# Performance work log

Measured on AMD Instinct MI355X. Metric: run time of the kernel, lower is better.

## Reference

```python
import jax, jax.numpy as jnp
import numpy as np
from jax import lax

# config (matches init_kwargs)
A, M, S, SR, L = 4, 32, 48000, 48000, 16000
NB = 8        # len(f_range)
BIN = 64      # alpha/beta bins (hardcoded in original)
TWO_PI = 2.0 * np.pi
NON_LINEAR_RATE = 0.3   # forward arg non_linear_rate
NOISE_RATE = 0.0        # forward arg noise_rate -> noise branch is a no-op
LOG10 = np.float32(np.log(10.0))

F_VALUES = jnp.asarray(np.geomspace(20.0, 8000.0, NB), jnp.float32)
ALPHA_VALUES = jnp.asarray(np.exp(np.linspace(np.log(3.0 / 10.0), np.log(3.0 * 100.0), BIN)), jnp.float32)
BETA_VALUES = jnp.asarray(np.exp(np.linspace(np.log(1e-9 / 10.0), np.log(1e-9 * 100.0), BIN)), jnp.float32)


def weighted_sum(params, values):
    # softplus -> normalize over last dim -> convex-ish combination of `values`
    x = jax.nn.softplus(params)
    x = x / x.sum(axis=-1, keepdims=True)
    return (x * values).sum(axis=-1)


def modified_sigmoid(x):
    # DDSP-style modified sigmoid used by DirectValue
    return 2.0 * jax.nn.sigmoid(x) ** LOG10 + 1e-7


def setup_inputs() -> dict:
    key = jax.random.key(0)
    ks = jax.random.split(key, 6)
    u = lambda k, shape, lo, hi: jax.random.uniform(k, shape, jnp.float32, lo, hi)
    return {
        "freq_lin_p": u(ks[0], (1, M, 1, NB), -4.0, 4.0),
        "freq_nl_p": u(ks[1], (A, M, S, NB), -4.0, 4.0),
        "alpha_p": u(ks[2], (1, M, 1, BIN), -4.0, 4.0),
        "beta_p": u(ks[3], (1, M, 1, BIN), -4.0, 4.0),
        "amp_v": u(ks[4], (A, M, 1), 0.0, 0.04),
        "forces": jax.random.normal(ks[5], (A, L), jnp.float32),
    }


def reference(freq_lin_p, freq_nl_p, alpha_p, beta_p, amp_v, forces):
    amp = modified_sigmoid(amp_v)                                   # [A,M,1]
    f_lin = weighted_sum(freq_lin_p, F_VALUES)                      # [1,M,1]
    undamped = f_lin + NON_LINEAR_RATE * weighted_sum(freq_nl_p, F_VALUES)  # [A,M,S]
    lbd = (undamped * TWO_PI) ** 2                                  # [A,M,S]
    alpha = weighted_sum(alpha_p, ALPHA_VALUES)                     # [1,M,1]
    beta = weighted_sum(beta_p, BETA_VALUES)                        # [1,M,1]
    damp = 0.5 * (alpha + beta * lbd)                               # [A,M,S]
    freq = jnp.sqrt(lbd - damp ** 2) / TWO_PI                       # [A,M,S]
    cum_damp = jnp.cumsum(damp / SR, axis=2)
    cum_freq = jnp.cumsum(freq / SR, axis=2)
    signal = (amp * jnp.exp(-cum_damp) * jnp.sin(TWO_PI * cum_freq)).sum(axis=1)  # [A,S]
    # grouped conv1d with time-flipped forces == full convolution with forces
    kernel = jnp.flip(forces, axis=-1)[:, None, :]                  # [A,1,L] (OIH)
    out = lax.conv_general_dilated(
        signal[None],                                               # [1,A,S]
        kernel,
        window_strides=(1,),
        padding=[(L - 1, L - 1)],
        feature_group_count=A,
        dimension_numbers=("NCH", "OIH", "NCH"),
    )
    out = out[0, :, :S]                                             # [A,S]
    return out  # + noise * NOISE_RATE (NOISE_RATE == 0)
```

## Files before the change

kernel.cpp:

```cpp
#include <hip/hip_runtime.h>
#include <hip/hip_bf16.h>
#include <math.h>

#define A_ 4
#define M_ 32
#define S_ 48000
#define L_ 16000
#define NB_ 8
#define BIN_ 64
#define TWO_PI_F 6.28318530717958647692f
#define INV_SR (1.0f / 48000.0f)
#define NCHUNK 47
#define NROW 128
#define SBPAD 16000
#define SBLEN 64256
#define SB_PLANE 257024
#define NKT 501
#define FB_PLANE 1026048u
#define UT_PER_A 188

#define CST_OFF    0u
#define SIG_OFF    1024u
#define PART_OFF   769024u
#define SIGBF_OFF  865280u
#define FRAGB_OFF  1893376u
#define WS_NEEDED  5997568u

typedef __attribute__((ext_vector_type(8))) short bf16x8;
typedef __attribute__((ext_vector_type(4))) float f32x4;

__device__ __forceinline__ float softplusf(float x) {
    float t = __expf(-fabsf(x));
    return fmaxf(x, 0.f) + __logf(1.f + t);
}
__device__ __forceinline__ unsigned short bfbits(float v) {
    __hip_bfloat16 h = __float2bfloat16(v);
    return *(unsigned short*)&h;
}
__device__ __forceinline__ float bf2f(unsigned short u) {
    unsigned x = ((unsigned)u) << 16;
    return *(float*)&x;
}

__global__ void k_precompute(const float* __restrict__ flin_p,
                             const float* __restrict__ alpha_p,
                             const float* __restrict__ beta_p,
                             const float* __restrict__ amp_v,
                             float* __restrict__ cst) {
    __shared__ float sF[NB_], sA[BIN_], sB[BIN_];
    int tid = threadIdx.x;
    if (tid < NB_) {
        double lf = log(20.0) + (double)tid * ((log(8000.0) - log(20.0)) / 7.0);
        float v = (float)exp(lf);
        sF[tid] = v; cst[tid] = v;
    }
    if (tid < BIN_) {
        double la = log(0.3) + (double)tid * ((log(300.0) - log(0.3)) / 63.0);
        sA[tid] = (float)exp(la);
        double lb = log(1e-10) + (double)tid * ((log(1e-7) - log(1e-10)) / 63.0);
        sB[tid] = (float)exp(lb);
    }
    __syncthreads();
    if (tid < M_) {
        float sum = 0.f, dot = 0.f;
        for (int i = 0; i < NB_; ++i) {
            float sp = softplusf(flin_p[tid * NB_ + i]);
            sum += sp; dot = fmaf(sp, sF[i], dot);
        }
        cst[8 + tid] = dot / sum;
        sum = 0.f; dot = 0.f;
        for (int i = 0; i < BIN_; ++i) {
            float sp = softplusf(alpha_p[tid * BIN_ + i]);
            sum += sp; dot = fmaf(sp, sA[i], dot);
        }
        cst[40 + tid] = dot / sum;
        sum = 0.f; dot = 0.f;
        for (int i = 0; i < BIN_; ++i) {
            float sp = softplusf(beta_p[tid * BIN_ + i]);
            sum += sp; dot = fmaf(sp, sB[i], dot);
        }
        cst[72 + tid] = dot / sum;
    }
    if (tid < A_ * M_) {
        float x = amp_v[tid];
        float sg = 1.f / (1.f + __expf(-x));
        cst[104 + tid] = 2.f * __expf(2.30258509299404568402f * __logf(sg)) + 1e-7f;
    }
}

__global__ __launch_bounds__(256) void k_fragB(const float* __restrict__ forces,
                                               unsigned short* __restrict__ fragB) {
    int t = blockIdx.x * 256 + threadIdx.x;
    if (t >= A_ * NKT * 64) return;
    int l  = t & 63;
    int kk = (t >> 6) % NKT;
    int a  = t / (NKT * 64);
    int v  = l & 15, hq = l >> 4;
    unsigned short hi[8], lo[8];
#pragma unroll
    for (int j = 0; j < 8; ++j) {
        int k = hq * 8 + j;
        int r = k & 15, hw = k >> 4;
        int fj = 32 * kk + 16 * hw + v - r;
        float fv = (fj >= 0 && fj < L_) ? forces[a * L_ + fj] : 0.f;
        hi[j] = bfbits(fv);
        lo[j] = bfbits(fv - bf2f(hi[j]));
    }
    uint4 ph, pl;
    ph.x = (unsigned)hi[0] | ((unsigned)hi[1] << 16);
    ph.y = (unsigned)hi[2] | ((unsigned)hi[3] << 16);
    ph.z = (unsigned)hi[4] | ((unsigned)hi[5] << 16);
    ph.w = (unsigned)hi[6] | ((unsigned)hi[7] << 16);
    pl.x = (unsigned)lo[0] | ((unsigned)lo[1] << 16);
    pl.y = (unsigned)lo[2] | ((unsigned)lo[3] << 16);
    pl.z = (unsigned)lo[4] | ((unsigned)lo[5] << 16);
    pl.w = (unsigned)lo[6] | ((unsigned)lo[7] << 16);
    ((uint4*)fragB)[t] = ph;
    ((uint4*)fragB)[FB_PLANE / 8 + t] = pl;
}

__device__ __forceinline__ void inc_partials(const float4* __restrict__ nl4,
                                             const float* __restrict__ cst,
                                             int row, int s0,
                                             float* lpx, float* lpy,
                                             float& rx, float& ry) {
    int m = row & 31;
    float Fv[8];
#pragma unroll
    for (int i = 0; i < 8; ++i) Fv[i] = cst[i];
    float flin = cst[8 + m], al = cst[40 + m], be = cst[72 + m];
    rx = 0.f; ry = 0.f;
#pragma unroll
    for (int k = 0; k < 4; ++k) {
        int s = s0 + k;
        float vx = 0.f, vy = 0.f;
        if (s < S_) {
            size_t off = ((size_t)row * S_ + s) * 2;
            float4 x0 = nl4[off];
            float4 x1 = nl4[off + 1];
            float xs[8] = {x0.x, x0.y, x0.z, x0.w, x1.x, x1.y, x1.z, x1.w};
            float sum = 0.f, dot = 0.f;
#pragma unroll
            for (int i = 0; i < 8; ++i) {
                float sp = softplusf(xs[i]);
                sum += sp; dot = fmaf(sp, Fv[i], dot);
            }
            float und = flin + 0.3f * (dot / sum);
            float w = TWO_PI_F * und;
            float lbd = w * w;
            float damp = 0.5f * fmaf(be, lbd, al);
            float freq = sqrtf(lbd - damp * damp) * (1.0f / TWO_PI_F);
            vx = damp * INV_SR;
            vy = freq * INV_SR;
        }
        rx += vx; lpx[k] = rx;
        ry += vy; lpy[k] = ry;
    }
}

__global__ __launch_bounds__(256) void k_sum(const float* __restrict__ nl,
                                             const float* __restrict__ cst,
                                             double2* __restrict__ part) {
    int chunk = blockIdx.x, row = blockIdx.y, tid = threadIdx.x;
    float lpx[4], lpy[4], rx, ry;
    inc_partials((const float4*)nl, cst, row, chunk * 1024 + tid * 4, lpx, lpy, rx, ry);

    __shared__ double rd[256], rf[256];
    rd[tid] = (double)rx; rf[tid] = (double)ry;
    __syncthreads();
    for (int o = 128; o > 0; o >>= 1) {
        if (tid < o) { rd[tid] += rd[tid + o]; rf[tid] += rf[tid + o]; }
        __syncthreads();
    }
    if (tid == 0) {
        double2 p; p.x = rd[0]; p.y = rf[0];
        part[row * NCHUNK + chunk] = p;
    }
}

__global__ void k_phase2(double2* __restrict__ part) {
    int r = threadIdx.x;
    if (r < NROW) {
        double cx = 0.0, cy = 0.0;
        for (int c = 0; c < NCHUNK; ++c) {
            double2 t = part[r * NCHUNK + c];
            double2 e; e.x = cx; e.y = cy;
            part[r * NCHUNK + c] = e;
            cx += t.x; cy += t.y;
        }
    }
}

__global__ __launch_bounds__(256) void k_eval(const float* __restrict__ nl,
                                              const float* __restrict__ cst,
                                              const double2* __restrict__ part,
                                              float* __restrict__ sig) {
    int chunk = blockIdx.x, row = blockIdx.y, tid = threadIdx.x;
    int a = row >> 5;
    int s0 = chunk * 1024 + tid * 4;
    float lpx[4], lpy[4], rx, ry;
    inc_partials((const float4*)nl, cst, row, s0, lpx, lpy, rx, ry);

    double2 carry = part[row * NCHUNK + chunk];
    float amp = cst[104 + row];

    __shared__ double sx[256], sy[256];
    sx[tid] = (double)rx; sy[tid] = (double)ry;
    __syncthreads();
    for (int o = 1; o < 256; o <<= 1) {
        double ax = (tid >= o) ? sx[tid - o] : 0.0;
        double ay = (tid >= o) ? sy[tid - o] : 0.0;
        __syncthreads();
        sx[tid] += ax; sy[tid] += ay;
        __syncthreads();
    }
    double ex = ((tid > 0) ? sx[tid - 1] : 0.0) + carry.x;
    double ey = ((tid > 0) ? sy[tid - 1] : 0.0) + carry.y;

#pragma unroll
    for (int k = 0; k < 4; ++k) {
        int s = s0 + k;
        if (s < S_) {
            double cd = ex + (double)lpx[k];
            if (cd < 16.0) {
                double cf = ey + (double)lpy[k];
                float ph = (float)(cf - floor(cf));
                float val = amp * __expf(-(float)cd) * __sinf(TWO_PI_F * ph);
                atomicAdd(&sig[a * S_ + s], val);
            }
        }
    }
}

__global__ __launch_bounds__(256) void k_convert(const float* __restrict__ sig,
                                                 unsigned short* __restrict__ sigbf) {
    int i = blockIdx.x * 256 + threadIdx.x;
    if (i >= A_ * SBLEN) return;
    int a = i / SBLEN, p = i - a * SBLEN;
    int s = p - SBPAD;
    float v = (s >= 0 && s < S_) ? sig[a * S_ + s] : 0.f;
    unsigned short hi = bfbits(v);
    sigbf[i] = hi;
    sigbf[SB_PLANE + i] = bfbits(v - bf2f(hi));
}

__global__ __launch_bounds__(512) void k_conv(const unsigned short* __restrict__ sigbf,
                                              const unsigned short* __restrict__ fragB,
                                              float* __restrict__ out) {
    int tile = blockIdx.x;
    int a = tile / UT_PER_A, ut = tile - a * UT_PER_A;
    int u0 = ut * 16;
    int tid = threadIdx.x;
    int wv = tid >> 6;
    int l  = tid & 63;
    int du = l & 15, hq = l >> 4, hw = hq >> 1, hr = hq & 1;

    int nkk = (u0 >> 1) + 9;
    if (nkk > NKT) nkk = NKT;

    const unsigned short* sH = sigbf + (size_t)a * SBLEN;
    const unsigned short* sL = sH + SB_PLANE;
    int ebase = SBPAD + 16 * (u0 + du) - 16 * hw + 8 * hr;
    const unsigned short* fH = fragB + (((size_t)a * NKT) * 64 + l) * 8;
    const unsigned short* fL = fH + FB_PLANE;

    f32x4 acc0 = {0.f, 0.f, 0.f, 0.f};
    f32x4 acc1 = {0.f, 0.f, 0.f, 0.f};

    for (int kk = wv; kk < nkk; kk += 16) {
        {
            int e = ebase - 32 * kk;
            bf16x8 ah = *(const bf16x8*)(sH + e);
            bf16x8 al = *(const bf16x8*)(sL + e);
            bf16x8 bh = *(const bf16x8*)(fH + (size_t)kk * 512);
            bf16x8 bl = *(const bf16x8*)(fL + (size_t)kk * 512);
            acc0 = __builtin_amdgcn_mfma_f32_16x16x32_bf16(ah, bh, acc0, 0, 0, 0);
            acc0 = __builtin_amdgcn_mfma_f32_16x16x32_bf16(al, bh, acc0, 0, 0, 0);
            acc0 = __builtin_amdgcn_mfma_f32_16x16x32_bf16(ah, bl, acc0, 0, 0, 0);
        }
        int k2 = kk + 8;
        if (k2 < nkk) {
            int e = ebase - 32 * k2;
            bf16x8 ah = *(const bf16x8*)(sH + e);
            bf16x8 al = *(const bf16x8*)(sL + e);
            bf16x8 bh = *(const bf16x8*)(fH + (size_t)k2 * 512);
            bf16x8 bl = *(const bf16x8*)(fL + (size_t)k2 * 512);
            acc1 = __builtin_amdgcn_mfma_f32_16x16x32_bf16(ah, bh, acc1, 0, 0, 0);
            acc1 = __builtin_amdgcn_mfma_f32_16x16x32_bf16(al, bh, acc1, 0, 0, 0);
            acc1 = __builtin_amdgcn_mfma_f32_16x16x32_bf16(ah, bl, acc1, 0, 0, 0);
        }
    }
    acc0 = acc0 + acc1;

    __shared__ float red[8][256];
#pragma unroll
    for (int r = 0; r < 4; ++r)
        red[wv][(hq * 4 + r) * 16 + (l & 15)] = acc0[r];
    __syncthreads();

    if (tid < 256) {
        float s = 0.f;
#pragma unroll
        for (int w2 = 0; w2 < 8; ++w2) s += red[w2][tid];
        int t = u0 * 16 + tid;
        if (t < S_) out[(size_t)a * S_ + t] = s;
    }
}

extern "C" void kernel_launch(void* const* d_in, const int* in_sizes, int n_in,
                              void* d_out, int out_size, void* d_ws, size_t ws_size,
                              hipStream_t stream) {
    if (ws_size < (size_t)WS_NEEDED) return;

    const float* flin_p  = (const float*)d_in[0];
    const float* nl_p    = (const float*)d_in[1];
    const float* alpha_p = (const float*)d_in[2];
    const float* beta_p  = (const float*)d_in[3];
    const float* amp_v   = (const float*)d_in[4];
    const float* forces  = (const float*)d_in[5];
    float* out = (float*)d_out;

    char* ws = (char*)d_ws;
    float*          cst    = (float*)(ws + CST_OFF);
    float*          sig    = (float*)(ws + SIG_OFF);
    double2*        part   = (double2*)(ws + PART_OFF);
    unsigned short* sigbf  = (unsigned short*)(ws + SIGBF_OFF);
    unsigned short* fragB  = (unsigned short*)(ws + FRAGB_OFF);

    hipMemsetAsync(sig, 0, (size_t)A_ * S_ * sizeof(float), stream);

    hipLaunchKernelGGL(k_precompute, dim3(1), dim3(256), 0, stream,
                       flin_p, alpha_p, beta_p, amp_v, cst);
    hipLaunchKernelGGL(k_fragB, dim3(501), dim3(256), 0, stream, forces, fragB);
    hipLaunchKernelGGL(k_sum, dim3(NCHUNK, NROW), dim3(256), 0, stream,
                       nl_p, cst, part);
    hipLaunchKernelGGL(k_phase2, dim3(1), dim3(128), 0, stream, part);
    hipLaunchKernelGGL(k_eval, dim3(NCHUNK, NROW), dim3(256), 0, stream,
                       nl_p, cst, part, sig);
    hipLaunchKernelGGL(k_convert, dim3(1004), dim3(256), 0, stream, sig, sigbf);
    hipLaunchKernelGGL(k_conv, dim3(A_ * UT_PER_A), dim3(512), 0, stream,
                       sigbf, fragB, out);
}
```

Before: 446.8 us.

## Fuse scan into single-pass decoupled lookback, drop split-bf16, retile conv

Result: slower. 1.022 ms (+128.7%).

```diff
diff --git a/kernel.cpp b/kernel.cpp
--- a/kernel.cpp
+++ b/kernel.cpp
@@ -14,17 +14,20 @@
 #define NROW 128
 #define SBPAD 16000
 #define SBLEN 64256
-#define SB_PLANE 257024
 #define NKT 501
-#define FB_PLANE 1026048u
-#define UT_PER_A 188
+#define MB_ 64
+#define CB_PER_A 47
 
 #define CST_OFF    0u
 #define SIG_OFF    1024u
-#define PART_OFF   769024u
-#define SIGBF_OFF  865280u
-#define FRAGB_OFF  1893376u
-#define WS_NEEDED  5997568u
+#define SIGBF_OFF  769024u
+#define FRAGB_OFF  1283072u
+#define FLAG_OFF   3335168u
+#define AGGD_OFF   3359232u
+#define AGGF_OFF   3407360u
+#define INCLD_OFF  3455488u
+#define INCLF_OFF  3503616u
+#define WS_NEEDED  3551744u
 
 typedef __attribute__((ext_vector_type(8))) short bf16x8;
 typedef __attribute__((ext_vector_type(4))) float f32x4;
@@ -36,10 +39,6 @@
 __device__ __forceinline__ unsigned short bfbits(float v) {
     __hip_bfloat16 h = __float2bfloat16(v);
     return *(unsigned short*)&h;
-}
-__device__ __forceinline__ float bf2f(unsigned short u) {
-    unsigned x = ((unsigned)u) << 16;
-    return *(float*)&x;
 }
 
 __global__ void k_precompute(const float* __restrict__ flin_p,
@@ -96,7 +95,7 @@
     int kk = (t >> 6) % NKT;
     int a  = t / (NKT * 64);
     int v  = l & 15, hq = l >> 4;
-    unsigned short hi[8], lo[8];
+    unsigned short hi[8];
 #pragma unroll
     for (int j = 0; j < 8; ++j) {
         int k = hq * 8 + j;
@@ -104,32 +103,34 @@
         int fj = 32 * kk + 16 * hw + v - r;
         float fv = (fj >= 0 && fj < L_) ? forces[a * L_ + fj] : 0.f;
         hi[j] = bfbits(fv);
-        lo[j] = bfbits(fv - bf2f(hi[j]));
-    }
-    uint4 ph, pl;
+    }
+    uint4 ph;
     ph.x = (unsigned)hi[0] | ((unsigned)hi[1] << 16);
     ph.y = (unsigned)hi[2] | ((unsigned)hi[3] << 16);
     ph.z = (unsigned)hi[4] | ((unsigned)hi[5] << 16);
     ph.w = (unsigned)hi[6] | ((unsigned)hi[7] << 16);
-    pl.x = (unsigned)lo[0] | ((unsigned)lo[1] << 16);
-    pl.y = (unsigned)lo[2] | ((unsigned)lo[3] << 16);
-    pl.z = (unsigned)lo[4] | ((unsigned)lo[5] << 16);
-    pl.w = (unsigned)lo[6] | ((unsigned)lo[7] << 16);
     ((uint4*)fragB)[t] = ph;
-    ((uint4*)fragB)[FB_PLANE / 8 + t] = pl;
-}
-
-__device__ __forceinline__ void inc_partials(const float4* __restrict__ nl4,
-                                             const float* __restrict__ cst,
-                                             int row, int s0,
-                                             float* lpx, float* lpy,
-                                             float& rx, float& ry) {
-    int m = row & 31;
+}
+
+__global__ __launch_bounds__(256) void k_scan(const float* __restrict__ nl,
+                                              const float* __restrict__ cst,
+                                              float* __restrict__ sig,
+                                              double* aggd, double* aggf,
+                                              double* incld, double* inclf,
+                                              int* flags) {
+    int chunk = blockIdx.x, row = blockIdx.y, tid = threadIdx.x;
+    int m = row & 31, a = row >> 5;
+
     float Fv[8];
 #pragma unroll
     for (int i = 0; i < 8; ++i) Fv[i] = cst[i];
     float flin = cst[8 + m], al = cst[40 + m], be = cst[72 + m];
-    rx = 0.f; ry = 0.f;
+    float amp = cst[104 + row];
+
+    const float4* nl4 = (const float4*)nl;
+    int s0 = chunk * 1024 + tid * 4;
+    float lpx[4], lpy[4];
+    float rx = 0.f, ry = 0.f;
 #pragma unroll
     for (int k = 0; k < 4; ++k) {
         int s = s0 + k;
@@ -156,55 +157,9 @@
         rx += vx; lpx[k] = rx;
         ry += vy; lpy[k] = ry;
     }
-}
-
-__global__ __launch_bounds__(256) void k_sum(const float* __restrict__ nl,
-                                             const float* __restrict__ cst,
-                                             double2* __restrict__ part) {
-    int chunk = blockIdx.x, row = blockIdx.y, tid = threadIdx.x;
-    float lpx[4], lpy[4], rx, ry;
-    inc_partials((const float4*)nl, cst, row, chunk * 1024 + tid * 4, lpx, lpy, rx, ry);
-
-    __shared__ double rd[256], rf[256];
-    rd[tid] = (double)rx; rf[tid] = (double)ry;
-    __syncthreads();
-    for (int o = 128; o > 0; o >>= 1) {
-        if (tid < o) { rd[tid] += rd[tid + o]; rf[tid] += rf[tid + o]; }
-        __syncthreads();
-    }
-    if (tid == 0) {
-        double2 p; p.x = rd[0]; p.y = rf[0];
-        part[row * NCHUNK + chunk] = p;
-    }
-}
-
-__global__ void k_phase2(double2* __restrict__ part) {
-    int r = threadIdx.x;
-    if (r < NROW) {
-        double cx = 0.0, cy = 0.0;
-        for (int c = 0; c < NCHUNK; ++c) {
-            double2 t = part[r * NCHUNK + c];
-            double2 e; e.x = cx; e.y = cy;
-            part[r * NCHUNK + c] = e;
-            cx += t.x; cy += t.y;
-        }
-    }
-}
-
-__global__ __launch_bounds__(256) void k_eval(const float* __restrict__ nl,
-                                              const float* __restrict__ cst,
-                                              const double2* __restrict__ part,
-                                              float* __restrict__ sig) {
-    int chunk = blockIdx.x, row = blockIdx.y, tid = threadIdx.x;
-    int a = row >> 5;
-    int s0 = chunk * 1024 + tid * 4;
-    float lpx[4], lpy[4], rx, ry;
-    inc_partials((const float4*)nl, cst, row, s0, lpx, lpy, rx, ry);
-
-    double2 carry = part[row * NCHUNK + chunk];
-    float amp = cst[104 + row];
 
     __shared__ double sx[256], sy[256];
+    __shared__ double sPd, sPf;
     sx[tid] = (double)rx; sy[tid] = (double)ry;
     __syncthreads();
     for (int o = 1; o < 256; o <<= 1) {
@@ -214,9 +169,42 @@
         sx[tid] += ax; sy[tid] += ay;
         __syncthreads();
     }
-    double ex = ((tid > 0) ? sx[tid - 1] : 0.0) + carry.x;
-    double ey = ((tid > 0) ? sy[tid - 1] : 0.0) + carry.y;
-
+
+    if (tid == 0) {
+        int idx = row * NCHUNK + chunk;
+        double Td = sx[255], Tf = sy[255];
+        double Pd = 0.0, Pf = 0.0;
+        if (chunk == 0) {
+            __hip_atomic_store(&incld[idx], Td, __ATOMIC_RELAXED, __HIP_MEMORY_SCOPE_AGENT);
+            __hip_atomic_store(&inclf[idx], Tf, __ATOMIC_RELAXED, __HIP_MEMORY_SCOPE_AGENT);
+            __hip_atomic_store(&flags[idx], 2, __ATOMIC_RELEASE, __HIP_MEMORY_SCOPE_AGENT);
+        } else {
+            __hip_atomic_store(&aggd[idx], Td, __ATOMIC_RELAXED, __HIP_MEMORY_SCOPE_AGENT);
+            __hip_atomic_store(&aggf[idx], Tf, __ATOMIC_RELAXED, __HIP_MEMORY_SCOPE_AGENT);
+            __hip_atomic_store(&flags[idx], 1, __ATOMIC_RELEASE, __HIP_MEMORY_SCOPE_AGENT);
+            int i = idx - 1;
+            while (1) {
+                int fl = __hip_atomic_load(&flags[i], __ATOMIC_ACQUIRE, __HIP_MEMORY_SCOPE_AGENT);
+                if (fl == 0) { __builtin_amdgcn_s_sleep(1); continue; }
+                if (fl == 2) {
+                    Pd += __hip_atomic_load(&incld[i], __ATOMIC_RELAXED, __HIP_MEMORY_SCOPE_AGENT);
+                    Pf += __hip_atomic_load(&inclf[i], __ATOMIC_RELAXED, __HIP_MEMORY_SCOPE_AGENT);
+                    break;
+                }
+                Pd += __hip_atomic_load(&aggd[i], __ATOMIC_RELAXED, __HIP_MEMORY_SCOPE_AGENT);
+                Pf += __hip_atomic_load(&aggf[i], __ATOMIC_RELAXED, __HIP_MEMORY_SCOPE_AGENT);
+                --i;
+            }
+            __hip_atomic_store(&incld[idx], Pd + Td, __ATOMIC_RELAXED, __HIP_MEMORY_SCOPE_AGENT);
+            __hip_atomic_store(&inclf[idx], Pf + Tf, __ATOMIC_RELAXED, __HIP_MEMORY_SCOPE_AGENT);
+            __hip_atomic_store(&flags[idx], 2, __ATOMIC_RELEASE, __HIP_MEMORY_SCOPE_AGENT);
+        }
+        sPd = Pd; sPf = Pf;
+    }
+    __syncthreads();
+
+    double ex = sPd + ((tid > 0) ? sx[tid - 1] : 0.0);
+    double ey = sPf + ((tid > 0) ? sy[tid - 1] : 0.0);
 #pragma unroll
     for (int k = 0; k < 4; ++k) {
         int s = s0 + k;
@@ -239,70 +227,55 @@
     int a = i / SBLEN, p = i - a * SBLEN;
     int s = p - SBPAD;
     float v = (s >= 0 && s < S_) ? sig[a * S_ + s] : 0.f;
-    unsigned short hi = bfbits(v);
-    sigbf[i] = hi;
-    sigbf[SB_PLANE + i] = bfbits(v - bf2f(hi));
+    sigbf[i] = bfbits(v);
 }
 
 __global__ __launch_bounds__(512) void k_conv(const unsigned short* __restrict__ sigbf,
                                               const unsigned short* __restrict__ fragB,
                                               float* __restrict__ out) {
-    int tile = blockIdx.x;
-    int a = tile / UT_PER_A, ut = tile - a * UT_PER_A;
-    int u0 = ut * 16;
+    int a   = blockIdx.y;
+    int ub0 = blockIdx.x * MB_;
     int tid = threadIdx.x;
-    int wv = tid >> 6;
-    int l  = tid & 63;
+    int wv  = tid >> 6;
+    int l   = tid & 63;
     int du = l & 15, hq = l >> 4, hw = hq >> 1, hr = hq & 1;
 
-    int nkk = (u0 >> 1) + 9;
+    int nkk = (ub0 >> 1) + 33;
     if (nkk > NKT) nkk = NKT;
 
-    const unsigned short* sH = sigbf + (size_t)a * SBLEN;
-    const unsigned short* sL = sH + SB_PLANE;
-    int ebase = SBPAD + 16 * (u0 + du) - 16 * hw + 8 * hr;
-    const unsigned short* fH = fragB + (((size_t)a * NKT) * 64 + l) * 8;
-    const unsigned short* fL = fH + FB_PLANE;
-
-    f32x4 acc0 = {0.f, 0.f, 0.f, 0.f};
-    f32x4 acc1 = {0.f, 0.f, 0.f, 0.f};
-
-    for (int kk = wv; kk < nkk; kk += 16) {
-        {
-            int e = ebase - 32 * kk;
-            bf16x8 ah = *(const bf16x8*)(sH + e);
-            bf16x8 al = *(const bf16x8*)(sL + e);
-            bf16x8 bh = *(const bf16x8*)(fH + (size_t)kk * 512);
-            bf16x8 bl = *(const bf16x8*)(fL + (size_t)kk * 512);
-            acc0 = __builtin_amdgcn_mfma_f32_16x16x32_bf16(ah, bh, acc0, 0, 0, 0);
-            acc0 = __builtin_amdgcn_mfma_f32_16x16x32_bf16(al, bh, acc0, 0, 0, 0);
-            acc0 = __builtin_amdgcn_mfma_f32_16x16x32_bf16(ah, bl, acc0, 0, 0, 0);
-        }
-        int k2 = kk + 8;
-        if (k2 < nkk) {
-            int e = ebase - 32 * k2;
-            bf16x8 ah = *(const bf16x8*)(sH + e);
-            bf16x8 al = *(const bf16x8*)(sL + e);
-            bf16x8 bh = *(const bf16x8*)(fH + (size_t)k2 * 512);
-            bf16x8 bl = *(const bf16x8*)(fL + (size_t)k2 * 512);
-            acc1 = __builtin_amdgcn_mfma_f32_16x16x32_bf16(ah, bh, acc1, 0, 0, 0);
-            acc1 = __builtin_amdgcn_mfma_f32_16x16x32_bf16(al, bh, acc1, 0, 0, 0);
-            acc1 = __builtin_amdgcn_mfma_f32_16x16x32_bf16(ah, bl, acc1, 0, 0, 0);
-        }
-    }
-    acc0 = acc0 + acc1;
-
-    __shared__ float red[8][256];
-#pragma unroll
-    for (int r = 0; r < 4; ++r)
-        red[wv][(hq * 4 + r) * 16 + (l & 15)] = acc0[r];
+    const unsigned short* sig_a = sigbf + (size_t)a * SBLEN;
+    int ebase = SBPAD + 16 * (ub0 + du) - 16 * hw + 8 * hr;
+    const unsigned short* fB = fragB + (((size_t)a * NKT) * 64 + l) * 8;
+
+    f32x4 acc[4];
+#pragma unroll
+    for (int m = 0; m < 4; ++m) acc[m] = (f32x4){0.f, 0.f, 0.f, 0.f};
+
+    for (int kk = wv; kk < nkk; kk += 8) {
+        bf16x8 bh = *(const bf16x8*)(fB + (size_t)kk * 512);
+        int e = ebase - 32 * kk;
+#pragma unroll
+        for (int m = 0; m < 4; ++m) {
+            bf16x8 ah = *(const bf16x8*)(sig_a + e + 256 * m);
+            acc[m] = __builtin_amdgcn_mfma_f32_16x16x32_bf16(ah, bh, acc[m], 0, 0, 0);
+        }
+    }
+
+    __shared__ float red[8][1024];
+#pragma unroll
+    for (int m = 0; m < 4; ++m)
+#pragma unroll
+        for (int r = 0; r < 4; ++r)
+            red[wv][m * 256 + (hq * 4 + r) * 16 + (l & 15)] = acc[m][r];
     __syncthreads();
 
-    if (tid < 256) {
+#pragma unroll
+    for (int rep = 0; rep < 2; ++rep) {
+        int o = tid + rep * 512;
         float s = 0.f;
 #pragma unroll
-        for (int w2 = 0; w2 < 8; ++w2) s += red[w2][tid];
-        int t = u0 * 16 + tid;
+        for (int w2 = 0; w2 < 8; ++w2) s += red[w2][o];
+        int t = 16 * ub0 + o;
         if (t < S_) out[(size_t)a * S_ + t] = s;
     }
 }
@@ -323,21 +296,23 @@
     char* ws = (char*)d_ws;
     float*          cst    = (float*)(ws + CST_OFF);
     float*          sig    = (float*)(ws + SIG_OFF);
-    double2*        part   = (double2*)(ws + PART_OFF);
     unsigned short* sigbf  = (unsigned short*)(ws + SIGBF_OFF);
     unsigned short* fragB  = (unsigned short*)(ws + FRAGB_OFF);
+    int*            flags  = (int*)(ws + FLAG_OFF);
+    double*         aggd   = (double*)(ws + AGGD_OFF);
+    double*         aggf   = (double*)(ws + AGGF_OFF);
+    double*         incld  = (double*)(ws + INCLD_OFF);
+    double*         inclf  = (double*)(ws + INCLF_OFF);
 
     hipMemsetAsync(sig, 0, (size_t)A_ * S_ * sizeof(float), stream);
+    hipMemsetAsync(flags, 0, (size_t)NROW * NCHUNK * sizeof(int), stream);
 
     hipLaunchKernelGGL(k_precompute, dim3(1), dim3(256), 0, stream,
                        flin_p, alpha_p, beta_p, amp_v, cst);
     hipLaunchKernelGGL(k_fragB, dim3(501), dim3(256), 0, stream, forces, fragB);
-    hipLaunchKernelGGL(k_sum, dim3(NCHUNK, NROW), dim3(256), 0, stream,
-                       nl_p, cst, part);
-    hipLaunchKernelGGL(k_phase2, dim3(1), dim3(128), 0, stream, part);
-    hipLaunchKernelGGL(k_eval, dim3(NCHUNK, NROW), dim3(256), 0, stream,
-                       nl_p, cst, part, sig);
+    hipLaunchKernelGGL(k_scan, dim3(NCHUNK, NROW), dim3(256), 0, stream,
+                       nl_p, cst, sig, aggd, aggf, incld, inclf, flags);
     hipLaunchKernelGGL(k_convert, dim3(1004), dim3(256), 0, stream, sig, sigbf);
-    hipLaunchKernelGGL(k_conv, dim3(A_ * UT_PER_A), dim3(512), 0, stream,
+    hipLaunchKernelGGL(k_conv, dim3(CB_PER_A, A_), dim3(512), 0, stream,
                        sigbf, fragB, out);
 }
```
